# Kernel optimization log

Measured on AMD Instinct MI355X. Metric: run time of the kernel, lower is better.

Reference implementation:

```python
import jax, jax.numpy as jnp
import numpy as np

N = 50000   # nodes
E = 800000  # directed edges
D = 128     # input_channels


def _kaiming(key, shape):
    fan_in = shape[0]
    return jax.random.normal(key, shape, jnp.float32) * np.float32(np.sqrt(2.0 / fan_in))


def setup_inputs():
    key = jax.random.key(0)
    ks = jax.random.split(key, 8)
    x = jax.random.normal(ks[0], (N, D), jnp.float32)
    edge_index = jax.random.randint(ks[1], (2, E), 0, N, dtype=jnp.int32)
    return {
        "x": x,
        "edge_index": edge_index,
        "W_in": _kaiming(ks[2], (D, D)),      "b_in": jnp.zeros((D,), jnp.float32),
        "W1": _kaiming(ks[3], (D, 2 * D)),    "b1": jnp.zeros((2 * D,), jnp.float32),
        "W2": _kaiming(ks[4], (2 * D, D)),    "b2": jnp.zeros((D,), jnp.float32),
        "W3": _kaiming(ks[5], (D, D // 2)),   "b3": jnp.zeros((D // 2,), jnp.float32),
        "W_out": _kaiming(ks[6], (D // 2, 1)), "b_out": jnp.zeros((1,), jnp.float32),
    }


def _gcn_conv(x, src, dst, W, b, n):
    """PyG GCNConv: add self-loops, symmetric D^-1/2 (A+I) D^-1/2 normalization."""
    h = x @ W  # [n, out]
    loop = jnp.arange(n, dtype=src.dtype)
    s = jnp.concatenate([src, loop])  # message sources (x_j)
    d = jnp.concatenate([dst, loop])  # aggregation targets (x_i)
    deg = jax.ops.segment_sum(jnp.ones_like(d, jnp.float32), d, num_segments=n)
    dis = jnp.where(deg > 0, jax.lax.rsqrt(jnp.maximum(deg, 1.0)), 0.0)
    norm = dis[s] * dis[d]  # [E+n]
    msg = h[s] * norm[:, None]  # gather + scale
    out = jax.ops.segment_sum(msg, d, num_segments=n)  # scatter-add
    return out + b


def reference(x, edge_index, W_in, b_in, W1, b1, W2, b2, W3, b3, W_out, b_out):
    src, dst = edge_index[0], edge_index[1]
    n = x.shape[0]
    lrelu = lambda t: jax.nn.leaky_relu(t, 0.01)
    # dropout in eval mode (identity)
    h = lrelu(x @ W_in + b_in)
    h = lrelu(_gcn_conv(h, src, dst, W1, b1, n))
    h = lrelu(_gcn_conv(h, src, dst, W2, b2, n))
    h = lrelu(_gcn_conv(h, src, dst, W3, b3, n))
    return h @ W_out + b_out  # [n, 1]
```

## Files before the change

### kernel.cpp

```cpp
#include <hip/hip_runtime.h>


#define LRELU(v) ((v) > 0.f ? (v) : 0.01f * (v))

typedef __attribute__((ext_vector_type(8))) _Float16 half8;
typedef __attribute__((ext_vector_type(8))) float float8;
typedef __attribute__((ext_vector_type(4))) float floatx4;

constexpr int CAP = 64;

__global__ __launch_bounds__(256) void k_fillpad(const int* __restrict__ src,
                                                 const int* __restrict__ dst,
                                                 int* __restrict__ cnt,
                                                 unsigned short* __restrict__ pad,
                                                 int E) {
  const int e = blockIdx.x * 256 + threadIdx.x;
  if (e < E) {
    const int d = dst[e];
    const int pos = atomicAdd(&cnt[d], 1);
    if (pos < CAP) pad[(long)d * CAP + pos] = (unsigned short)src[e];
  }
}

__global__ __launch_bounds__(256) void k_wtall(const float* __restrict__ W_in,
                                               const float* __restrict__ W1,
                                               const float* __restrict__ W2,
                                               const float* __restrict__ W3,
                                               _Float16* __restrict__ wt_in,
                                               _Float16* __restrict__ wt1,
                                               _Float16* __restrict__ wt2,
                                               _Float16* __restrict__ wt3) {
  const int idx = blockIdx.x * 256 + threadIdx.x;
  const int m = blockIdx.y;
  if (m == 0) {
    if (idx < 128 * 128) {
      const int k = idx >> 7, f = idx & 127;
      wt_in[f * 128 + k] = (_Float16)W_in[idx];
    }
  } else if (m == 1) {
    if (idx < 128 * 256) {
      const int k = idx >> 8, f = idx & 255;
      wt1[f * 128 + k] = (_Float16)W1[idx];
    }
  } else if (m == 2) {
    if (idx < 256 * 128) {
      const int k = idx >> 7, f = idx & 127;
      wt2[f * 256 + k] = (_Float16)W2[idx];
    }
  } else {
    if (idx < 128 * 64) {
      const int k = idx >> 6, f = idx & 63;
      wt3[f * 128 + k] = (_Float16)W3[idx];
    }
  }
}

template <int K, int F, int EPI, typename IT>
__global__ __launch_bounds__(256) void k_gemm(const IT* __restrict__ X,
                                              const _Float16* __restrict__ Wt,
                                              const float* __restrict__ b,
                                              const int* __restrict__ cnt,
                                              _Float16* __restrict__ out, int M) {
  constexpr int TM = 64;
  constexpr int PAD = 8;
  constexpr int LK = K + PAD;
  constexpr int CW = F / 4;
  constexpr int NT = CW / 16;
  constexpr int NK = K / 32;
  __shared__ _Float16 xs[TM * LK];

  const int m0 = blockIdx.x * TM;
  const int tid = threadIdx.x;
  const int w = tid >> 6;
  const int lane = tid & 63;
  const int m = lane & 15;
  const int q = lane >> 4;

  half8 breg[NT][NK];
#pragma unroll
  for (int t = 0; t < NT; ++t)
#pragma unroll
    for (int kc = 0; kc < NK; ++kc)
      breg[t][kc] =
          *(const half8*)&Wt[(long)(w * CW + t * 16 + m) * K + kc * 32 + q * 8];

  constexpr int CPR = K / 8;
  for (int idx = tid; idx < TM * CPR; idx += 256) {
    const int row = idx / CPR;
    const int kk = idx % CPR;
    const int g = m0 + row;
    half8 h = (half8)(_Float16)0.f;
    if (g < M) {
      if constexpr (sizeof(IT) == 4) {
        const float4* p = (const float4*)&X[(long)g * K + kk * 8];
        float4 a = p[0], c = p[1];
        h[0] = (_Float16)a.x; h[1] = (_Float16)a.y;
        h[2] = (_Float16)a.z; h[3] = (_Float16)a.w;
        h[4] = (_Float16)c.x; h[5] = (_Float16)c.y;
        h[6] = (_Float16)c.z; h[7] = (_Float16)c.w;
      } else {
        h = *(const half8*)&X[(long)g * K + kk * 8];
      }
    }
    *(half8*)&xs[row * LK + kk * 8] = h;
  }
  __syncthreads();

  floatx4 acc[4][NT];
#pragma unroll
  for (int rt = 0; rt < 4; ++rt)
#pragma unroll
    for (int t = 0; t < NT; ++t) acc[rt][t] = (floatx4){0.f, 0.f, 0.f, 0.f};

#pragma unroll
  for (int kc = 0; kc < NK; ++kc) {
    half8 af[4];
#pragma unroll
    for (int rt = 0; rt < 4; ++rt)
      af[rt] = *(const half8*)&xs[(rt * 16 + m) * LK + kc * 32 + q * 8];
#pragma unroll
    for (int rt = 0; rt < 4; ++rt)
#pragma unroll
      for (int t = 0; t < NT; ++t)
        acc[rt][t] = __builtin_amdgcn_mfma_f32_16x16x32_f16(af[rt], breg[t][kc],
                                                            acc[rt][t], 0, 0, 0);
  }

#pragma unroll
  for (int rt = 0; rt < 4; ++rt) {
#pragma unroll
    for (int r = 0; r < 4; ++r) {
      const int row = m0 + rt * 16 + q * 4 + r;
      if (row < M) {
        const float dv = rsqrtf((float)cnt[row] + 1.0f);
#pragma unroll
        for (int t = 0; t < NT; ++t) {
          const int col = w * CW + t * 16 + m;
          float v = acc[rt][t][r];
          if constexpr (EPI == 0) { v += b[col]; v = LRELU(v); v *= dv; }
          if constexpr (EPI == 2) { v *= dv; }
          out[(long)row * F + col] = (_Float16)v;
        }
      }
    }
  }
}

__global__ __launch_bounds__(256) void k_gemm2x(const _Float16* __restrict__ X,
                                                const _Float16* __restrict__ Wt1,
                                                const float* __restrict__ b1,
                                                const _Float16* __restrict__ Wt2,
                                                const int* __restrict__ cnt,
                                                _Float16* __restrict__ out,
                                                int M) {
  constexpr int TM = 64;
  constexpr int LK1 = 128 + 8;
  constexpr int LK2 = 256 + 8;
  __shared__ _Float16 xs[TM * LK1];
  __shared__ _Float16 ys[TM * LK2];

  const int m0 = blockIdx.x * TM;
  const int tid = threadIdx.x;
  const int w = tid >> 6;
  const int lane = tid & 63;
  const int m = lane & 15;
  const int q = lane >> 4;

  for (int idx = tid; idx < TM * 16; idx += 256) {
    const int row = idx >> 4;
    const int kk = idx & 15;
    const int g = m0 + row;
    half8 h = (half8)(_Float16)0.f;
    if (g < M) h = *(const half8*)&X[(long)g * 128 + kk * 8];
    *(half8*)&xs[row * LK1 + kk * 8] = h;
  }

  half8 breg1[4][4];
#pragma unroll
  for (int t = 0; t < 4; ++t)
#pragma unroll
    for (int kc = 0; kc < 4; ++kc)
      breg1[t][kc] =
          *(const half8*)&Wt1[(long)(w * 64 + t * 16 + m) * 128 + kc * 32 + q * 8];

  __syncthreads();

  floatx4 acc1[4][4];
#pragma unroll
  for (int rt = 0; rt < 4; ++rt)
#pragma unroll
    for (int t = 0; t < 4; ++t) acc1[rt][t] = (floatx4){0.f, 0.f, 0.f, 0.f};

#pragma unroll
  for (int kc = 0; kc < 4; ++kc) {
    half8 af[4];
#pragma unroll
    for (int rt = 0; rt < 4; ++rt)
      af[rt] = *(const half8*)&xs[(rt * 16 + m) * LK1 + kc * 32 + q * 8];
#pragma unroll
    for (int rt = 0; rt < 4; ++rt)
#pragma unroll
      for (int t = 0; t < 4; ++t)
        acc1[rt][t] = __builtin_amdgcn_mfma_f32_16x16x32_f16(af[rt], breg1[t][kc],
                                                             acc1[rt][t], 0, 0, 0);
  }

#pragma unroll
  for (int rt = 0; rt < 4; ++rt) {
#pragma unroll
    for (int r = 0; r < 4; ++r) {
      const int row = rt * 16 + q * 4 + r;
#pragma unroll
      for (int t = 0; t < 4; ++t) {
        const int col = w * 64 + t * 16 + m;
        float v = acc1[rt][t][r] + b1[col];
        ys[row * LK2 + col] = (_Float16)LRELU(v);
      }
    }
  }

  half8 breg2[2][8];
#pragma unroll
  for (int t = 0; t < 2; ++t)
#pragma unroll
    for (int kc = 0; kc < 8; ++kc)
      breg2[t][kc] =
          *(const half8*)&Wt2[(long)(w * 32 + t * 16 + m) * 256 + kc * 32 + q * 8];

  __syncthreads();

  floatx4 acc2[4][2];
#pragma unroll
  for (int rt = 0; rt < 4; ++rt)
#pragma unroll
    for (int t = 0; t < 2; ++t) acc2[rt][t] = (floatx4){0.f, 0.f, 0.f, 0.f};

#pragma unroll
  for (int kc = 0; kc < 8; ++kc) {
    half8 af[4];
#pragma unroll
    for (int rt = 0; rt < 4; ++rt)
      af[rt] = *(const half8*)&ys[(rt * 16 + m) * LK2 + kc * 32 + q * 8];
#pragma unroll
    for (int rt = 0; rt < 4; ++rt)
#pragma unroll
      for (int t = 0; t < 2; ++t)
        acc2[rt][t] = __builtin_amdgcn_mfma_f32_16x16x32_f16(af[rt], breg2[t][kc],
                                                             acc2[rt][t], 0, 0, 0);
  }

#pragma unroll
  for (int rt = 0; rt < 4; ++rt) {
#pragma unroll
    for (int r = 0; r < 4; ++r) {
      const int row = m0 + rt * 16 + q * 4 + r;
      if (row < M) {
        const float dv = rsqrtf((float)cnt[row] + 1.0f);
#pragma unroll
        for (int t = 0; t < 2; ++t) {
          const int col = w * 32 + t * 16 + m;
          out[(long)row * 128 + col] = (_Float16)(acc2[rt][t][r] * dv);
        }
      }
    }
  }
}

template <int F, int MODE>
__global__ __launch_bounds__(256) void k_agg(const _Float16* __restrict__ G,
                                             const unsigned short* __restrict__ pad,
                                             const int* __restrict__ cnt,
                                             const float* __restrict__ b,
                                             const float* __restrict__ Wout,
                                             const float* __restrict__ bout,
                                             void* __restrict__ out, int N) {
  const int w = threadIdx.x >> 6;
  const int lane = threadIdx.x & 63;
  const int c = lane & 7;
  const int j = lane >> 3;
  const int n = j >> 2;
  const int jj = j & 3;
  const int i0 = blockIdx.x * 8 + w * 2;
  int i = i0 + n;
  const bool valid = (i < N);
  if (!valid) i = N - 1;
  const int col0 = (F == 128) ? ((int)blockIdx.y << 6) : 0;

  const _Float16* gbase = G + col0 + c * 8;
  const int cn = min(cnt[i], CAP);
  const unsigned short* plist = pad + (long)i * CAP;

  float8 acc = {0.f, 0.f, 0.f, 0.f, 0.f, 0.f, 0.f, 0.f};
  if (jj == 0)
    acc = __builtin_convertvector(*(const half8*)(gbase + (long)i * F), float8);
  for (int e = jj; e < cn; e += 4) {
    const int s = plist[e];
    acc += __builtin_convertvector(*(const half8*)(gbase + (long)s * F), float8);
  }
#pragma unroll
  for (int k = 0; k < 8; ++k) {
    acc[k] += __shfl_xor(acc[k], 8);
    acc[k] += __shfl_xor(acc[k], 16);
  }

  const float dv = rsqrtf((float)cnt[i] + 1.0f);
  if constexpr (MODE == 2) {
    float p = 0.f;
#pragma unroll
    for (int k = 0; k < 8; ++k) {
      const int col = c * 8 + k;
      float v = acc[k] * dv + b[col];
      v = LRELU(v);
      p += v * Wout[col];
    }
    p += __shfl_xor(p, 1);
    p += __shfl_xor(p, 2);
    p += __shfl_xor(p, 4);
    if (valid && jj == 0 && c == 0) ((float*)out)[i] = p + bout[0];
  } else {
    if (valid && jj == 0) {
      half8 hv;
#pragma unroll
      for (int k = 0; k < 8; ++k) {
        float v = acc[k] * dv;
        if constexpr (MODE == 1) { v += b[col0 + c * 8 + k]; v = LRELU(v); }
        hv[k] = (_Float16)v;
      }
      *(half8*)&((_Float16*)out)[(long)i * F + col0 + c * 8] = hv;
    }
  }
}


extern "C" void kernel_launch(void* const* d_in, const int* in_sizes, int n_in,
                              void* d_out, int out_size, void* d_ws, size_t ws_size,
                              hipStream_t stream) {
  const float* x     = (const float*)d_in[0];
  const int* eidx    = (const int*)d_in[1];
  const float* W_in  = (const float*)d_in[2];
  const float* b_in  = (const float*)d_in[3];
  const float* W1    = (const float*)d_in[4];
  const float* b1    = (const float*)d_in[5];
  const float* W2    = (const float*)d_in[6];
  const float* b2    = (const float*)d_in[7];
  const float* W3    = (const float*)d_in[8];
  const float* b3    = (const float*)d_in[9];
  const float* W_out = (const float*)d_in[10];
  const float* b_out = (const float*)d_in[11];
  float* out = (float*)d_out;

  const int N = in_sizes[0] / 128;
  const int E = in_sizes[1] / 2;
  const int* src = eidx;
  const int* dst = eidx + E;

  size_t off = 0;
  char* base = (char*)d_ws;
  auto alloc = [&](size_t bytes) -> void* {
    void* p = base + off;
    off = (off + bytes + 255) & ~(size_t)255;
    return p;
  };
  int* cnt            = (int*)alloc((size_t)N * sizeof(int));
  unsigned short* pad = (unsigned short*)alloc((size_t)N * CAP * 2);
  _Float16* wt_in     = (_Float16*)alloc((size_t)128 * 128 * 2);
  _Float16* wt1       = (_Float16*)alloc((size_t)256 * 128 * 2);
  _Float16* wt2       = (_Float16*)alloc((size_t)128 * 256 * 2);
  _Float16* wt3       = (_Float16*)alloc((size_t)64 * 128 * 2);
  _Float16* buf1      = (_Float16*)alloc((size_t)N * 128 * 2);
  _Float16* buf2      = (_Float16*)alloc((size_t)N * 128 * 2);
  _Float16* buf3      = (_Float16*)alloc((size_t)N * 64 * 2);

  hipMemsetAsync(cnt, 0, (size_t)N * sizeof(int), stream);

  const int gE = (E + 255) / 256;
  const int gRows = (N + 63) / 64;
  const int gAggP = (N + 7) / 8;

  k_wtall<<<dim3(128, 4), 256, 0, stream>>>(W_in, W1, W2, W3,
                                            wt_in, wt1, wt2, wt3);
  k_fillpad<<<gE, 256, 0, stream>>>(src, dst, cnt, pad, E);

  k_gemm<128, 128, 0, float><<<gRows, 256, 0, stream>>>(x, wt_in, b_in, cnt,
                                                        buf1, N);
  k_agg<128, 0><<<dim3(gAggP, 2), 256, 0, stream>>>(buf1, pad, cnt, nullptr,
                                                    nullptr, nullptr, buf2, N);
  k_gemm2x<<<gRows, 256, 0, stream>>>(buf2, wt1, b1, wt2, cnt, buf1, N);
  k_agg<128, 1><<<dim3(gAggP, 2), 256, 0, stream>>>(buf1, pad, cnt, b2,
                                                    nullptr, nullptr, buf2, N);
  k_gemm<128, 64, 2, _Float16><<<gRows, 256, 0, stream>>>(buf2, wt3, nullptr,
                                                          cnt, buf3, N);
  k_agg<64, 2><<<gAggP, 256, 0, stream>>>(buf3, pad, cnt, b3,
                                          W_out, b_out, out, N);
}
```

Baseline: 285.9 us.

## Merge weight conversion and edge bucketing into one range-partitioned prep kernel

Combines the weight transpose/convert kernel and the edge padding kernel into a single launch. The edge part now splits destinations into 8 node ranges: each edge chunk is read by 8 blocks, and each block only does the atomics and pad writes for destinations in its own range. This is meant to localize the atomics and scattered pad writes to a smaller address window for better cache/L2 locality, and it removes one launch. The cost is reading dst 8 times and launching 8x more blocks, plus an integer division per edge.

```diff
diff --git a/kernel.cpp b/kernel.cpp
--- a/kernel.cpp
+++ b/kernel.cpp
@@ -9,48 +9,57 @@
 
 constexpr int CAP = 64;
 
-__global__ __launch_bounds__(256) void k_fillpad(const int* __restrict__ src,
-                                                 const int* __restrict__ dst,
-                                                 int* __restrict__ cnt,
-                                                 unsigned short* __restrict__ pad,
-                                                 int E) {
-  const int e = blockIdx.x * 256 + threadIdx.x;
-  if (e < E) {
-    const int d = dst[e];
-    const int pos = atomicAdd(&cnt[d], 1);
-    if (pos < CAP) pad[(long)d * CAP + pos] = (unsigned short)src[e];
-  }
-}
-
-__global__ __launch_bounds__(256) void k_wtall(const float* __restrict__ W_in,
-                                               const float* __restrict__ W1,
-                                               const float* __restrict__ W2,
-                                               const float* __restrict__ W3,
-                                               _Float16* __restrict__ wt_in,
-                                               _Float16* __restrict__ wt1,
-                                               _Float16* __restrict__ wt2,
-                                               _Float16* __restrict__ wt3) {
-  const int idx = blockIdx.x * 256 + threadIdx.x;
-  const int m = blockIdx.y;
-  if (m == 0) {
-    if (idx < 128 * 128) {
-      const int k = idx >> 7, f = idx & 127;
-      wt_in[f * 128 + k] = (_Float16)W_in[idx];
-    }
-  } else if (m == 1) {
-    if (idx < 128 * 256) {
-      const int k = idx >> 8, f = idx & 255;
-      wt1[f * 128 + k] = (_Float16)W1[idx];
-    }
-  } else if (m == 2) {
-    if (idx < 256 * 128) {
-      const int k = idx >> 7, f = idx & 127;
-      wt2[f * 256 + k] = (_Float16)W2[idx];
+__global__ __launch_bounds__(256) void k_prep(const int* __restrict__ src,
+                                              const int* __restrict__ dst,
+                                              int* __restrict__ cnt,
+                                              unsigned short* __restrict__ pad,
+                                              const float* __restrict__ W_in,
+                                              const float* __restrict__ W1,
+                                              const float* __restrict__ W2,
+                                              const float* __restrict__ W3,
+                                              _Float16* __restrict__ wt_in,
+                                              _Float16* __restrict__ wt1,
+                                              _Float16* __restrict__ wt2,
+                                              _Float16* __restrict__ wt3,
+                                              int E, int PR) {
+  const int b = blockIdx.x;
+  const int tid = threadIdx.x;
+  if (b < 128) {
+    const int m = b >> 5;
+    const int blk = b & 31;
+    const int idx = blk * 256 + tid;
+    if (m == 0) {
+      for (int i = idx; i < 128 * 128; i += 8192) {
+        const int k = i >> 7, f = i & 127;
+        wt_in[f * 128 + k] = (_Float16)W_in[i];
+      }
+    } else if (m == 1) {
+      for (int i = idx; i < 128 * 256; i += 8192) {
+        const int k = i >> 8, f = i & 255;
+        wt1[f * 128 + k] = (_Float16)W1[i];
+      }
+    } else if (m == 2) {
+      for (int i = idx; i < 256 * 128; i += 8192) {
+        const int k = i >> 7, f = i & 127;
+        wt2[f * 256 + k] = (_Float16)W2[i];
+      }
+    } else {
+      for (int i = idx; i < 128 * 64; i += 8192) {
+        const int k = i >> 6, f = i & 63;
+        wt3[f * 128 + k] = (_Float16)W3[i];
+      }
     }
   } else {
-    if (idx < 128 * 64) {
-      const int k = idx >> 6, f = idx & 63;
-      wt3[f * 128 + k] = (_Float16)W3[idx];
+    const int bb = b - 128;
+    const int range = bb & 7;
+    const int chunk = bb >> 3;
+    const int e = chunk * 256 + tid;
+    if (e < E) {
+      const int d = dst[e];
+      if (d / PR == range) {
+        const int pos = atomicAdd(&cnt[d], 1);
+        if (pos < CAP) pad[(long)d * CAP + pos] = (unsigned short)src[e];
+      }
     }
   }
 }
@@ -353,6 +362,7 @@
   const int E = in_sizes[1] / 2;
   const int* src = eidx;
   const int* dst = eidx + E;
+  const int PR = (N + 7) / 8;
 
   size_t off = 0;
   char* base = (char*)d_ws;
@@ -377,9 +387,9 @@
   const int gRows = (N + 63) / 64;
   const int gAggP = (N + 7) / 8;
 
-  k_wtall<<<dim3(128, 4), 256, 0, stream>>>(W_in, W1, W2, W3,
-                                            wt_in, wt1, wt2, wt3);
-  k_fillpad<<<gE, 256, 0, stream>>>(src, dst, cnt, pad, E);
+  k_prep<<<128 + 8 * gE, 256, 0, stream>>>(src, dst, cnt, pad,
+                                           W_in, W1, W2, W3,
+                                           wt_in, wt1, wt2, wt3, E, PR);
 
   k_gemm<128, 128, 0, float><<<gRows, 256, 0, stream>>>(x, wt_in, b_in, cnt,
                                                         buf1, N);
```

After: 273.8 us. 4.2% less time.
